# Performance work log

Hardware: AMD Instinct MI355X
Metric: run time of the kernel (lower is better)

The kernel has to match this reference:

```python
import jax, jax.numpy as jnp
import numpy as np

REGION_INDEX = [[3,0,1,2,4],[7,8,9,10,11],[5,6],[13,12],[14,15,23,24,32,33],[22,21,31,30,40,39],[16,17,18,19,20],[25,26,27,28,29],[34,35,36,37,38],[41,42],[49,48],[43,44,45,46,47],[50,51,57],[56,55,61],[52,53,54],[58,59,60]]
INPUT_SIZE = 5
HIDDEN = 100
REGIONS = 16


def setup_inputs() -> dict:
    key = jax.random.key(0)
    ks = jax.random.split(key, 5)
    features = jax.random.normal(ks[0], (128, 256, 62, INPUT_SIZE), dtype=jnp.float32)
    s = 1.0 / np.sqrt(HIDDEN)  # PyTorch LSTM init scale
    # dir 0 = forward, dir 1 = reverse
    w_ih = jax.random.uniform(ks[1], (REGIONS, 2, 4 * HIDDEN, INPUT_SIZE), jnp.float32, -s, s)
    w_hh = jax.random.uniform(ks[2], (REGIONS, 2, 4 * HIDDEN, HIDDEN), jnp.float32, -s, s)
    b_ih = jax.random.uniform(ks[3], (REGIONS, 2, 4 * HIDDEN), jnp.float32, -s, s)
    b_hh = jax.random.uniform(ks[4], (REGIONS, 2, 4 * HIDDEN), jnp.float32, -s, s)
    return {"features": features, "w_ih": w_ih, "w_hh": w_hh, "b_ih": b_ih, "b_hh": b_hh}


def _lstm_last(x, Wih, Whh, bih, bhh):
    # x: (N, L, I) -> final hidden state h_{L-1}: (N, H). PyTorch gate order i,f,g,o.
    N = x.shape[0]
    H = Whh.shape[1]
    bias = bih + bhh

    def step(carry, xt):
        h, c = carry
        g = xt @ Wih.T + h @ Whh.T + bias
        i, f, gg, o = jnp.split(g, 4, axis=-1)
        c = jax.nn.sigmoid(f) * c + jax.nn.sigmoid(i) * jnp.tanh(gg)
        h = jax.nn.sigmoid(o) * jnp.tanh(c)
        return (h, c), None

    h0 = jnp.zeros((N, H), x.dtype)
    (h, _), _ = jax.lax.scan(step, (h0, h0), jnp.swapaxes(x, 0, 1))
    return h


def _forward(features, w_ih, w_hh, b_ih, b_hh):
    # flatten (B, T, 62, 5) -> (N, 62, 5)
    x = features.reshape(-1, features.shape[2], features.shape[3])
    outs = []
    for r in range(REGIONS):
        idx = jnp.asarray(REGION_INDEX[r])
        xr = x[:, idx, :]  # (N, L_r, 5)
        # forward-direction hidden at last timestep
        h_f = _lstm_last(xr, w_ih[r, 0], w_hh[r, 0], b_ih[r, 0], b_hh[r, 0])
        # reverse-direction output at last position == one step on x[:, -1] from zero state
        h_b = _lstm_last(xr[:, -1:, :], w_ih[r, 1], w_hh[r, 1], b_ih[r, 1], b_hh[r, 1])
        outs.append(jnp.concatenate([h_f, h_b], axis=-1))  # (N, 2H)
    return jnp.stack(outs, axis=1)  # (N, 16, 2H)


def reference(features, w_ih, w_hh, b_ih, b_hh):
    return _forward(features, w_ih, w_hh, b_ih, b_hh)
```

## Files before the change

kernel.cpp:

```cpp
#include <hip/hip_runtime.h>


typedef _Float16 f16;
typedef _Float16 half8 __attribute__((ext_vector_type(8)));
typedef float floatx4 __attribute__((ext_vector_type(4)));

#define FEAT_STRIDE 310
#define WST 136

__constant__ int c_pos[16][6] = {
 {3,0,1,2,4,0},{7,8,9,10,11,0},{5,6,0,0,0,0},{13,12,0,0,0,0},
 {14,15,23,24,32,33},{22,21,31,30,40,39},{16,17,18,19,20,0},{25,26,27,28,29,0},
 {34,35,36,37,38,0},{41,42,0,0,0,0},{49,48,0,0,0,0},{43,44,45,46,47,0},
 {50,51,57,0,0,0},{56,55,61,0,0,0},{52,53,54,0,0,0},{58,59,60,0,0,0}};
__constant__ int c_len[16] = {5,5,2,2,6,6,5,5,5,2,2,5,3,3,3,3};

__device__ __forceinline__ float sigf(float x) {
  return __builtin_amdgcn_rcpf(1.f + __builtin_amdgcn_exp2f(-1.44269504088896f * x));
}
__device__ __forceinline__ float tanhf_fast(float x) {
  return 1.f - 2.f * __builtin_amdgcn_rcpf(1.f + __builtin_amdgcn_exp2f(2.88539008177793f * x));
}

__global__ __launch_bounds__(256) void prep_kernel(
    const float* __restrict__ w_ih, const float* __restrict__ w_hh,
    const float* __restrict__ b_ih, const float* __restrict__ b_hh,
    f16* __restrict__ wp)
{
  int id = blockIdx.x * 256 + threadIdx.x;
  if (id >= 16 * 400 * 128) return;
  int k = id & 127;
  int rowN = (id >> 7) % 400;
  int r = (id >> 7) / 400;
  int j = rowN >> 2, g = rowN & 3;
  int orig = (r * 2 + 0) * 400 + g * 100 + j;
  float v;
  if (k < 100)       v = w_hh[orig * 100 + k];
  else if (k < 105)  v = w_ih[orig * 5 + (k - 100)];
  else if (k == 105) v = b_ih[orig] + b_hh[orig];
  else               v = 0.f;
  wp[id] = (f16)v;
}

__global__ __launch_bounds__(512, 2) void fwd_kernel(
    const float* __restrict__ feat, const f16* __restrict__ wp,
    float* __restrict__ out)
{
  __shared__ __align__(16) unsigned char lds_raw[158976];
  f16*   Wl = (f16*)lds_raw;
  f16*   Sl = (f16*)(lds_raw + 108800);
  float* Xl = (float*)(lds_raw + 143616);

  const int bx = blockIdx.x;
  const int r  = bx >> 8;
  const int n0 = (bx & 255) << 7;
  const int tid  = threadIdx.x;
  const int wave = tid >> 6;
  const int lane = tid & 63;
  const int quad = lane >> 4;
  const int l15  = lane & 15;
  const int T = c_len[r];

  {
    const f16* wr = wp + (size_t)r * 400 * 128;
    for (int idx = tid; idx < 400 * 16; idx += 512) {
      int row = idx >> 4, c = idx & 15;
      *(half8*)(Wl + row * WST + 8 * c) = *(const half8*)(wr + row * 128 + 8 * c);
    }
  }
  for (int idx = tid; idx < T * 640; idx += 512) {
    int t = idx / 640, rem = idx - t * 640;
    int m = rem / 5, s = rem - m * 5;
    Xl[idx] = feat[(size_t)(n0 + m) * FEAT_STRIDE + c_pos[r][t] * 5 + s];
  }
  {
    unsigned int* Swd = (unsigned int*)Sl;
    for (int idx = tid; idx < 8 * 16 * (WST / 2); idx += 512) {
      int kw = idx % (WST / 2);
      Swd[idx] = (kw == 52) ? 0x3C000000u : 0u;
    }
  }
  __syncthreads();

  f16* Sw = Sl + wave * 16 * WST;
  const int xm = lane >> 2, xsl = lane & 3;

  float creg[25];
  #pragma unroll
  for (int tn = 0; tn < 25; ++tn) creg[tn] = 0.f;

  for (int t = 0; t < T; ++t) {
    Sw[xm * WST + 100 + xsl] = (f16)Xl[t * 640 + (wave * 16 + xm) * 5 + xsl];
    if (lane < 16)
      Sw[l15 * WST + 104] = (f16)Xl[t * 640 + (wave * 16 + l15) * 5 + 4];

    half8 bf[4];
    #pragma unroll
    for (int kf = 0; kf < 4; ++kf)
      bf[kf] = *(const half8*)(Sw + l15 * WST + 32 * kf + 8 * quad);

    const bool last = (t + 1 == T);
    #pragma unroll
    for (int tn = 0; tn < 25; ++tn) {
      floatx4 acc = {0.f, 0.f, 0.f, 0.f};
      #pragma unroll
      for (int kf = 0; kf < 4; ++kf) {
        half8 wfr = *(const half8*)(Wl + (16 * tn + l15) * WST + 32 * kf + 8 * quad);
        acc = __builtin_amdgcn_mfma_f32_16x16x32_f16(wfr, bf[kf], acc, 0, 0, 0);
      }
      float ig = sigf(acc[0]);
      float fg = sigf(acc[1]);
      float gg = tanhf_fast(acc[2]);
      float og = sigf(acc[3]);
      float cn = fg * creg[tn] + ig * gg;
      creg[tn] = cn;
      float hv = og * tanhf_fast(cn);
      int j = 4 * tn + quad;
      if (!last) {
        Sw[l15 * WST + j] = (f16)hv;
      } else {
        out[(size_t)(n0 + wave * 16 + l15) * 3200 + r * 200 + j] = hv;
      }
    }
  }
}

__global__ __launch_bounds__(256) void bwd_kernel(
    const float* __restrict__ feat, const float* __restrict__ w_ih,
    const float* __restrict__ b_ih, const float* __restrict__ b_hh,
    float* __restrict__ out)
{
  __shared__ float wg[300 * 7];
  __shared__ float xs[128 * 5];
  const int bx = blockIdx.x;
  const int r  = bx >> 8;
  const int n0 = (bx & 255) << 7;
  const int tid = threadIdx.x;
  const int pos = c_pos[r][c_len[r] - 1];

  for (int i = tid; i < 2100; i += 256) {
    int row = i / 7, c = i - row * 7;
    int q = row / 100, jj = row - q * 100;
    int qq = (q == 0) ? 0 : (q + 1);
    int orig = (r * 2 + 1) * 400 + qq * 100 + jj;
    float v = 0.f;
    if (c < 5)       v = w_ih[orig * 5 + c];
    else if (c == 5) v = b_ih[orig] + b_hh[orig];
    wg[i] = v;
  }
  for (int i = tid; i < 640; i += 256) {
    int nl = i / 5, s = i - nl * 5;
    xs[i] = feat[(size_t)(n0 + nl) * FEAT_STRIDE + pos * 5 + s];
  }
  __syncthreads();

  if (tid < 200) {
    const int g  = tid / 100;
    const int jj = tid - g * 100;
    const float* wi = wg + jj * 7;
    const float* wc = wg + (100 + jj) * 7;
    const float* wo = wg + (200 + jj) * 7;
    float i0 = wi[0], i1 = wi[1], i2 = wi[2], i3 = wi[3], i4 = wi[4], ib = wi[5];
    float c0 = wc[0], c1 = wc[1], c2 = wc[2], c3 = wc[3], c4 = wc[4], cb = wc[5];
    float o0 = wo[0], o1 = wo[1], o2 = wo[2], o3 = wo[3], o4 = wo[4], ob = wo[5];
    for (int i = 0; i < 64; ++i) {
      int nl = g * 64 + i;
      const float* xp = xs + nl * 5;
      float x0 = xp[0], x1 = xp[1], x2 = xp[2], x3 = xp[3], x4 = xp[4];
      float gi = ib + i0*x0 + i1*x1 + i2*x2 + i3*x3 + i4*x4;
      float gc = cb + c0*x0 + c1*x1 + c2*x2 + c3*x3 + c4*x4;
      float go = ob + o0*x0 + o1*x1 + o2*x2 + o3*x3 + o4*x4;
      float cc = sigf(gi) * tanhf_fast(gc);
      float hh = sigf(go) * tanhf_fast(cc);
      out[(size_t)(n0 + nl) * 3200 + r * 200 + 100 + jj] = hh;
    }
  }
}

extern "C" void kernel_launch(void* const* d_in, const int* in_sizes, int n_in,
                              void* d_out, int out_size, void* d_ws, size_t ws_size,
                              hipStream_t stream) {
  const float* feat = (const float*)d_in[0];
  const float* w_ih = (const float*)d_in[1];
  const float* w_hh = (const float*)d_in[2];
  const float* b_ih = (const float*)d_in[3];
  const float* b_hh = (const float*)d_in[4];
  float* out = (float*)d_out;
  f16* wp = (f16*)d_ws;

  prep_kernel<<<3200, 256, 0, stream>>>(w_ih, w_hh, b_ih, b_hh, wp);
  fwd_kernel<<<4096, 512, 0, stream>>>(feat, wp, out);
  bwd_kernel<<<4096, 256, 0, stream>>>(feat, w_ih, b_ih, b_hh, out);
}
```

Measured before the change: 947.7 us.

## Repack LSTM weights into compact swizzled LDS layout with 1024-thread blocks

```diff
diff --git a/kernel.cpp b/kernel.cpp
--- a/kernel.cpp
+++ b/kernel.cpp
@@ -2,11 +2,16 @@
 
 
 typedef _Float16 f16;
+typedef _Float16 half2v __attribute__((ext_vector_type(2)));
+typedef _Float16 half4v __attribute__((ext_vector_type(4)));
 typedef _Float16 half8 __attribute__((ext_vector_type(8)));
 typedef float floatx4 __attribute__((ext_vector_type(4)));
 
 #define FEAT_STRIDE 310
-#define WST 136
+
+#define LDS_WTAIL 76800
+#define LDS_SCR   89600
+#define SCR_WAVE  3584
 
 __constant__ int c_pos[16][6] = {
  {3,0,1,2,4,0},{7,8,9,10,11,0},{5,6,0,0,0,0},{13,12,0,0,0,0},
@@ -21,6 +26,10 @@
 __device__ __forceinline__ float tanhf_fast(float x) {
   return 1.f - 2.f * __builtin_amdgcn_rcpf(1.f + __builtin_amdgcn_exp2f(2.88539008177793f * x));
 }
+__device__ __forceinline__ half8 hzero8() {
+  half8 z = {(f16)0,(f16)0,(f16)0,(f16)0,(f16)0,(f16)0,(f16)0,(f16)0};
+  return z;
+}
 
 __global__ __launch_bounds__(256) void prep_kernel(
     const float* __restrict__ w_ih, const float* __restrict__ w_hh,
@@ -28,86 +37,115 @@
     f16* __restrict__ wp)
 {
   int id = blockIdx.x * 256 + threadIdx.x;
-  if (id >= 16 * 400 * 128) return;
-  int k = id & 127;
-  int rowN = (id >> 7) % 400;
-  int r = (id >> 7) / 400;
+  if (id >= 16 * 400 * 112) return;
+  int c = id % 112;
+  int rowN = (id / 112) % 400;
+  int r = id / (112 * 400);
   int j = rowN >> 2, g = rowN & 3;
   int orig = (r * 2 + 0) * 400 + g * 100 + j;
   float v;
-  if (k < 100)       v = w_hh[orig * 100 + k];
-  else if (k < 105)  v = w_ih[orig * 5 + (k - 100)];
-  else if (k == 105) v = b_ih[orig] + b_hh[orig];
-  else               v = 0.f;
+  if (c < 96) {
+    int k = 4 * (c % 24) + (c / 24);
+    v = w_hh[orig * 100 + k];
+  } else {
+    int tc = c - 96;
+    if (tc < 5)               v = w_ih[orig * 5 + tc];
+    else if (tc == 5)         v = b_ih[orig] + b_hh[orig];
+    else if (tc >= 8 && tc < 12) v = w_hh[orig * 100 + 96 + (tc - 8)];
+    else                      v = 0.f;
+  }
   wp[id] = (f16)v;
 }
 
-__global__ __launch_bounds__(512, 2) void fwd_kernel(
+__global__ __launch_bounds__(1024, 4) void fwd_kernel(
     const float* __restrict__ feat, const f16* __restrict__ wp,
     float* __restrict__ out)
 {
-  __shared__ __align__(16) unsigned char lds_raw[158976];
-  f16*   Wl = (f16*)lds_raw;
-  f16*   Sl = (f16*)(lds_raw + 108800);
-  float* Xl = (float*)(lds_raw + 143616);
+  __shared__ __align__(16) unsigned char lds[146944];
 
   const int bx = blockIdx.x;
-  const int r  = bx >> 8;
-  const int n0 = (bx & 255) << 7;
+  const int r  = bx >> 7;
+  const int n0 = (bx & 127) << 8;
   const int tid  = threadIdx.x;
   const int wave = tid >> 6;
   const int lane = tid & 63;
   const int quad = lane >> 4;
   const int l15  = lane & 15;
   const int T = c_len[r];
+  const int m_self = n0 + wave * 16 + l15;
 
   {
-    const f16* wr = wp + (size_t)r * 400 * 128;
-    for (int idx = tid; idx < 400 * 16; idx += 512) {
-      int row = idx >> 4, c = idx & 15;
-      *(half8*)(Wl + row * WST + 8 * c) = *(const half8*)(wr + row * 128 + 8 * c);
-    }
-  }
-  for (int idx = tid; idx < T * 640; idx += 512) {
-    int t = idx / 640, rem = idx - t * 640;
-    int m = rem / 5, s = rem - m * 5;
-    Xl[idx] = feat[(size_t)(n0 + m) * FEAT_STRIDE + c_pos[r][t] * 5 + s];
+    unsigned char* scr = lds + LDS_SCR + wave * SCR_WAVE;
+    for (int i = lane; i < SCR_WAVE / 16; i += 64) {
+      floatx4 z = {0.f, 0.f, 0.f, 0.f};
+      *(floatx4*)(scr + 16 * i) = z;
+    }
   }
   {
-    unsigned int* Swd = (unsigned int*)Sl;
-    for (int idx = tid; idx < 8 * 16 * (WST / 2); idx += 512) {
-      int kw = idx % (WST / 2);
-      Swd[idx] = (kw == 52) ? 0x3C000000u : 0u;
-    }
+    const f16* wr = wp + (size_t)r * 400 * 112;
+    for (int idx = tid; idx < 400 * 14; idx += 1024) {
+      int row = idx / 14, c = idx - row * 14;
+      half8 v = *(const half8*)(wr + row * 112 + 8 * c);
+      int sw = (row & 7) << 4;
+      int dst = (c < 12) ? ((row * 192 + c * 16) ^ sw)
+                         : (LDS_WTAIL + ((row * 32 + (c - 12) * 16) ^ sw));
+      *(half8*)(lds + dst) = v;
+    }
+  }
+  float nx0, nx1, nx2, nx3, nx4;
+  if (quad == 1) {
+    const float* fb = feat + (size_t)m_self * FEAT_STRIDE + c_pos[r][0] * 5;
+    nx0 = fb[0]; nx1 = fb[1]; nx2 = fb[2]; nx3 = fb[3]; nx4 = fb[4];
   }
   __syncthreads();
 
-  f16* Sw = Sl + wave * 16 * WST;
-  const int xm = lane >> 2, xsl = lane & 3;
+  unsigned char* Sm = lds + LDS_SCR + wave * SCR_WAVE;
+  unsigned char* St = Sm + 3072;
+  const int swz = (l15 & 7) << 4;
+
+  if (quad == 1) {
+    half4v xa; xa[0] = (f16)nx0; xa[1] = (f16)nx1; xa[2] = (f16)nx2; xa[3] = (f16)nx3;
+    half2v xb; xb[0] = (f16)nx4; xb[1] = (f16)1.0f;
+    *(half4v*)(St + ((l15 * 32) ^ swz)) = xa;
+    *(half2v*)(St + ((l15 * 32 + 8) ^ swz)) = xb;
+  }
 
   float creg[25];
   #pragma unroll
   for (int tn = 0; tn < 25; ++tn) creg[tn] = 0.f;
 
   for (int t = 0; t < T; ++t) {
-    Sw[xm * WST + 100 + xsl] = (f16)Xl[t * 640 + (wave * 16 + xm) * 5 + xsl];
-    if (lane < 16)
-      Sw[l15 * WST + 104] = (f16)Xl[t * 640 + (wave * 16 + l15) * 5 + 4];
-
-    half8 bf[4];
-    #pragma unroll
-    for (int kf = 0; kf < 4; ++kf)
-      bf[kf] = *(const half8*)(Sw + l15 * WST + 32 * kf + 8 * quad);
-
-    const bool last = (t + 1 == T);
+    const bool notlast = (t + 1 < T);
+
+    half8 bf0 = *(const half8*)(Sm + ((l15 * 192 +   0 + quad * 16) ^ swz));
+    half8 bf1 = *(const half8*)(Sm + ((l15 * 192 +  64 + quad * 16) ^ swz));
+    half8 bf2 = *(const half8*)(Sm + ((l15 * 192 + 128 + quad * 16) ^ swz));
+    half8 bf3 = hzero8();
+    if (quad < 2)
+      bf3 = *(const half8*)(St + ((l15 * 32 + quad * 16) ^ swz));
+
+    if (notlast && quad == 1) {
+      const float* fb = feat + (size_t)m_self * FEAT_STRIDE + c_pos[r][t + 1] * 5;
+      nx0 = fb[0]; nx1 = fb[1]; nx2 = fb[2]; nx3 = fb[3]; nx4 = fb[4];
+    }
+
     #pragma unroll
     for (int tn = 0; tn < 25; ++tn) {
+      const int rb = (16 * tn + l15) * 192;
+      const int tb = (16 * tn + l15) * 32;
+      half8 wf0 = *(const half8*)(lds + ((rb +   0 + quad * 16) ^ swz));
+      half8 wf1 = *(const half8*)(lds + ((rb +  64 + quad * 16) ^ swz));
+      half8 wf2 = *(const half8*)(lds + ((rb + 128 + quad * 16) ^ swz));
+      half8 wf3 = hzero8();
+      if (quad < 2)
+        wf3 = *(const half8*)(lds + LDS_WTAIL + ((tb + quad * 16) ^ swz));
+
       floatx4 acc = {0.f, 0.f, 0.f, 0.f};
-      #pragma unroll
-      for (int kf = 0; kf < 4; ++kf) {
-        half8 wfr = *(const half8*)(Wl + (16 * tn + l15) * WST + 32 * kf + 8 * quad);
-        acc = __builtin_amdgcn_mfma_f32_16x16x32_f16(wfr, bf[kf], acc, 0, 0, 0);
-      }
+      acc = __builtin_amdgcn_mfma_f32_16x16x32_f16(wf0, bf0, acc, 0, 0, 0);
+      acc = __builtin_amdgcn_mfma_f32_16x16x32_f16(wf1, bf1, acc, 0, 0, 0);
+      acc = __builtin_amdgcn_mfma_f32_16x16x32_f16(wf2, bf2, acc, 0, 0, 0);
+      acc = __builtin_amdgcn_mfma_f32_16x16x32_f16(wf3, bf3, acc, 0, 0, 0);
+
       float ig = sigf(acc[0]);
       float fg = sigf(acc[1]);
       float gg = tanhf_fast(acc[2]);
@@ -115,17 +153,28 @@
       float cn = fg * creg[tn] + ig * gg;
       creg[tn] = cn;
       float hv = og * tanhf_fast(cn);
-      int j = 4 * tn + quad;
-      if (!last) {
-        Sw[l15 * WST + j] = (f16)hv;
+
+      if (notlast) {
+        if (tn < 24) {
+          *(f16*)(Sm + ((l15 * 192 + (tn + 24 * quad) * 2) ^ swz)) = (f16)hv;
+        } else {
+          *(f16*)(St + ((l15 * 32 + 16 + 2 * quad) ^ swz)) = (f16)hv;
+        }
       } else {
-        out[(size_t)(n0 + wave * 16 + l15) * 3200 + r * 200 + j] = hv;
+        out[(size_t)m_self * 3200 + r * 200 + 4 * tn + quad] = hv;
       }
     }
-  }
-}
-
-__global__ __launch_bounds__(256) void bwd_kernel(
+
+    if (notlast && quad == 1) {
+      half4v xa; xa[0] = (f16)nx0; xa[1] = (f16)nx1; xa[2] = (f16)nx2; xa[3] = (f16)nx3;
+      half2v xb; xb[0] = (f16)nx4; xb[1] = (f16)1.0f;
+      *(half4v*)(St + ((l15 * 32) ^ swz)) = xa;
+      *(half2v*)(St + ((l15 * 32 + 8) ^ swz)) = xb;
+    }
+  }
+}
+
+__global__ __launch_bounds__(512) void bwd_kernel(
     const float* __restrict__ feat, const float* __restrict__ w_ih,
     const float* __restrict__ b_ih, const float* __restrict__ b_hh,
     float* __restrict__ out)
@@ -138,7 +187,7 @@
   const int tid = threadIdx.x;
   const int pos = c_pos[r][c_len[r] - 1];
 
-  for (int i = tid; i < 2100; i += 256) {
+  for (int i = tid; i < 2100; i += 512) {
     int row = i / 7, c = i - row * 7;
     int q = row / 100, jj = row - q * 100;
     int qq = (q == 0) ? 0 : (q + 1);
@@ -148,13 +197,13 @@
     else if (c == 5) v = b_ih[orig] + b_hh[orig];
     wg[i] = v;
   }
-  for (int i = tid; i < 640; i += 256) {
+  for (int i = tid; i < 640; i += 512) {
     int nl = i / 5, s = i - nl * 5;
     xs[i] = feat[(size_t)(n0 + nl) * FEAT_STRIDE + pos * 5 + s];
   }
   __syncthreads();
 
-  if (tid < 200) {
+  if (tid < 400) {
     const int g  = tid / 100;
     const int jj = tid - g * 100;
     const float* wi = wg + jj * 7;
@@ -163,8 +212,8 @@
     float i0 = wi[0], i1 = wi[1], i2 = wi[2], i3 = wi[3], i4 = wi[4], ib = wi[5];
     float c0 = wc[0], c1 = wc[1], c2 = wc[2], c3 = wc[3], c4 = wc[4], cb = wc[5];
     float o0 = wo[0], o1 = wo[1], o2 = wo[2], o3 = wo[3], o4 = wo[4], ob = wo[5];
-    for (int i = 0; i < 64; ++i) {
-      int nl = g * 64 + i;
+    for (int i = 0; i < 32; ++i) {
+      int nl = g * 32 + i;
       const float* xp = xs + nl * 5;
       float x0 = xp[0], x1 = xp[1], x2 = xp[2], x3 = xp[3], x4 = xp[4];
       float gi = ib + i0*x0 + i1*x1 + i2*x2 + i3*x3 + i4*x4;
@@ -188,7 +237,7 @@
   float* out = (float*)d_out;
   f16* wp = (f16*)d_ws;
 
-  prep_kernel<<<3200, 256, 0, stream>>>(w_ih, w_hh, b_ih, b_hh, wp);
-  fwd_kernel<<<4096, 512, 0, stream>>>(feat, wp, out);
-  bwd_kernel<<<4096, 256, 0, stream>>>(feat, w_ih, b_ih, b_hh, out);
-}
+  prep_kernel<<<2800, 256, 0, stream>>>(w_ih, w_hh, b_ih, b_hh, wp);
+  fwd_kernel<<<2048, 1024, 0, stream>>>(feat, wp, out);
+  bwd_kernel<<<4096, 512, 0, stream>>>(feat, w_ih, b_ih, b_hh, out);
+}
```

After: 1.372 ms. 44.8% more time.
